# Kernel optimization log

Measured on AMD Instinct MI355X. Metric: run time of the kernel, lower is better.

Reference implementation:

```python
import jax, jax.numpy as jnp
import numpy as np
from jax import lax

NPOINT, RADIUS, NSAMPLE, K_KEY = 64, 1.0, 32, 64

def conv1d(x, W, b):
    # 1x1 Conv1d: x [B,Cin,N], W [Cout,Cin], b [Cout] -> [B,Cout,N]
    return jnp.einsum('bcn,dc->bdn', x, W) + b[None, :, None]

def farthest_point_sample(xyz, npoint):
    # xyz [B,N,3] -> idx [B,npoint]
    B, N, _ = xyz.shape
    dist0 = jnp.full((B, N), 1e10, dtype=xyz.dtype)
    far0 = jnp.zeros((B,), dtype=jnp.int32)
    def body(carry, _):
        dist, far = carry
        centroid = jnp.take_along_axis(xyz, far[:, None, None].astype(jnp.int32), axis=1)  # [B,1,3]
        d = jnp.sum((xyz - centroid) ** 2, -1)
        dist = jnp.minimum(dist, d)
        nxt = jnp.argmax(dist, -1).astype(jnp.int32)
        return (dist, nxt), far
    _, idxs = lax.scan(body, (dist0, far0), None, length=npoint)
    return idxs.T  # [B,npoint]

def ball_query(radius, nsample, xyz, new_xyz):
    # xyz [B,N,3], new_xyz [B,S,3] -> group_idx [B,S,nsample]
    N = xyz.shape[1]
    sqr = jnp.sum((new_xyz[:, :, None, :] - xyz[:, None, :, :]) ** 2, -1)  # [B,S,N]
    gidx = jnp.where(sqr > radius ** 2, N, jnp.arange(N, dtype=jnp.int32)[None, None, :])
    gidx = jnp.sort(gidx, axis=-1)[..., :nsample]
    first = gidx[..., :1]
    gidx = jnp.where(gidx == N, first, gidx)
    return gidx

def sample_and_group(npoint, radius, nsample, xyz, points):
    # xyz [B,N,3], points [B,N,D]
    B = xyz.shape[0]
    fps_idx = farthest_point_sample(xyz, npoint)                     # [B,S]
    bidx = jnp.arange(B)[:, None]
    new_xyz = xyz[bidx, fps_idx]                                     # [B,S,3]
    gidx = ball_query(radius, nsample, xyz, new_xyz)                 # [B,S,ns]
    bidx2 = jnp.arange(B)[:, None, None]
    grouped_xyz = xyz[bidx2, gidx]                                   # [B,S,ns,3]
    grouped_xyz_norm = grouped_xyz - new_xyz[:, :, None, :]
    grouped_points = points[bidx2, gidx]                             # [B,S,ns,D]
    new_points = jnp.concatenate([grouped_xyz_norm, grouped_points], axis=-1)
    return new_xyz, new_points

def setup_inputs() -> dict:
    key = jax.random.key(0)
    ks = jax.random.split(key, 12)
    B, C, N = 8, 6, 65536
    def w(k, co, ci):
        return jax.random.normal(k, (co, ci), jnp.float32) * (1.0 / np.sqrt(ci))
    return {
        'src_pts': jax.random.normal(ks[0], (B, C, N), jnp.float32),
        'tgt_pts': jax.random.normal(ks[1], (B, C, N), jnp.float32),
        'W1': w(ks[2], 32, 6),  'b1': jnp.zeros((32,), jnp.float32),
        'W2': w(ks[3], 64, 32), 'b2': jnp.zeros((64,), jnp.float32),
        'Wa': w(ks[4], 16, 64), 'ba': jnp.zeros((16,), jnp.float32),
        'Wb': w(ks[5], 8, 16),  'bb': jnp.zeros((8,), jnp.float32),
        'Wc': w(ks[6], 1, 8),   'bc': jnp.zeros((1,), jnp.float32),
    }

def reference(src_pts, tgt_pts, W1, b1, W2, b2, Wa, ba, Wb, bb, Wc, bc):
    # feat_extraction_layer: 1x1 conv stack over points -> deep per-point features
    h = jax.nn.relu(conv1d(src_pts, W1, b1))            # [B,32,N]
    deep_feat_pts = jax.nn.relu(conv1d(h, W2, b2))      # [B,64,N]
    # weighting_layer: per-point saliency weight + top-k keypoint indices (1-D, batch-0 idiom)
    w = jax.nn.relu(conv1d(deep_feat_pts, Wa, ba))
    w = jax.nn.relu(conv1d(w, Wb, bb))
    w = jax.nn.softplus(conv1d(w, Wc, bc))              # [B,1,N]
    _, keypts_idx = lax.top_k(w[0, 0], K_KEY)           # [K]
    # irregular keypoint gather (shared index across batch, as in src_pts[:, :, idx])
    src_keypts = src_pts[:, :, keypts_idx].transpose(0, 2, 1)   # [B,K,C]
    # ball-query sample_and_group on keypoints (computed then discarded, as in original)
    _gxyz, _gpts = sample_and_group(NPOINT, RADIUS, NSAMPLE, src_keypts[:, :, :3], src_keypts[:, :, 3:])
    return src_keypts
```

## Files before the change

kernel.cpp:

```cpp
#include <hip/hip_runtime.h>
#include <stdint.h>

#define N_PTS 65536
#define NB1 32768
#define NB2 4096
#define CAND_CAP 4096
#define FCAP 1024
typedef unsigned long long u64;


__global__ __launch_bounds__(256) void zero_kernel(uint4* __restrict__ z, int n4)
{
    const int i = blockIdx.x * 256 + threadIdx.x;
    const uint4 zz = {0u, 0u, 0u, 0u};
    if (i < n4) z[i] = zz;
}

__global__ __launch_bounds__(128, 1) void score_kernel(
    const float* __restrict__ src,
    const float* __restrict__ W1, const float* __restrict__ b1,
    const float* __restrict__ W2, const float* __restrict__ b2,
    const float* __restrict__ Wa, const float* __restrict__ ba,
    const float* __restrict__ Wb, const float* __restrict__ bb,
    const float* __restrict__ Wc, const float* __restrict__ bc,
    float* __restrict__ scores, unsigned* __restrict__ hist1)
{
    __shared__ unsigned histL[NB1];
    __shared__ __align__(16) float sW1[32 * 8];
    __shared__ __align__(16) float sW2[64 * 32];
    __shared__ __align__(16) float sWaT[64 * 16];
    __shared__ __align__(16) float sWb[8 * 16];
    __shared__ float sb2[64], sba[16], sbb[8], sWc[8], sbc1[1];
    const int t = threadIdx.x;

    {
        uint4* h4 = (uint4*)histL;
        const uint4 zz = {0u, 0u, 0u, 0u};
        #pragma unroll
        for (int i = 0; i < 64; i++) h4[t + 128 * i] = zz;
    }
    for (int i = t; i < 256; i += 128) {
        const int j = i >> 3, c = i & 7;
        sW1[i] = (c < 6) ? W1[j * 6 + c] : ((c == 6) ? b1[j] : 0.f);
    }
    for (int i = t; i < 2048; i += 128) sW2[i] = W2[i];
    for (int i = t; i < 1024; i += 128) {
        const int j = i >> 4, q = i & 15;
        sWaT[i] = Wa[q * 64 + j];
    }
    if (t < 128) sWb[t] = Wb[t];
    if (t < 64)  sb2[t] = b2[t];
    if (t < 16)  sba[t] = ba[t];
    if (t < 8)   { sbb[t] = bb[t]; sWc[t] = Wc[t]; }
    if (t == 0)  sbc1[0] = bc[0];
    __syncthreads();

    const int base = blockIdx.x * 512;
    int p[4];
    #pragma unroll
    for (int P = 0; P < 4; P++) p[P] = base + 128 * P + t;

    float x[4][6];
    #pragma unroll
    for (int c = 0; c < 6; c++) {
        #pragma unroll
        for (int P = 0; P < 4; P++) x[P][c] = src[c * N_PTS + p[P]];
    }

    float h1[4][32];
    #pragma unroll 8
    for (int j = 0; j < 32; j++) {
        const float4 wA = *(const float4*)&sW1[j * 8];
        const float4 wB = *(const float4*)&sW1[j * 8 + 4];
        #pragma unroll
        for (int P = 0; P < 4; P++) {
            float a = wB.z;
            a = fmaf(wA.x, x[P][0], a); a = fmaf(wA.y, x[P][1], a);
            a = fmaf(wA.z, x[P][2], a); a = fmaf(wA.w, x[P][3], a);
            a = fmaf(wB.x, x[P][4], a); a = fmaf(wB.y, x[P][5], a);
            h1[P][j] = fmaxf(a, 0.f);
        }
    }

    float h3[4][16];
    #pragma unroll
    for (int q = 0; q < 16; q++) {
        const float b = sba[q];
        h3[0][q] = b; h3[1][q] = b; h3[2][q] = b; h3[3][q] = b;
    }

    #pragma unroll 2
    for (int j = 0; j < 64; j++) {
        const float4* w2r = (const float4*)&sW2[j * 32];
        const float4* war = (const float4*)&sWaT[j * 16];
        float4 w[8], wq[4];
        #pragma unroll
        for (int i = 0; i < 8; i++) w[i] = w2r[i];
        #pragma unroll
        for (int i = 0; i < 4; i++) wq[i] = war[i];
        const float bj = sb2[j];

        float v[4];
        #pragma unroll
        for (int P = 0; P < 4; P++) {
            float a0 = 0.f, a1 = 0.f, a2 = 0.f, a3 = 0.f;
            #pragma unroll
            for (int i4 = 0; i4 < 8; i4++) {
                a0 = fmaf(w[i4].x, h1[P][4 * i4 + 0], a0);
                a1 = fmaf(w[i4].y, h1[P][4 * i4 + 1], a1);
                a2 = fmaf(w[i4].z, h1[P][4 * i4 + 2], a2);
                a3 = fmaf(w[i4].w, h1[P][4 * i4 + 3], a3);
            }
            v[P] = fmaxf((a0 + a1) + (a2 + a3) + bj, 0.f);
        }
        #pragma unroll
        for (int q4 = 0; q4 < 4; q4++) {
            const float4 ww = wq[q4];
            #pragma unroll
            for (int P = 0; P < 4; P++) {
                h3[P][4 * q4 + 0] = fmaf(ww.x, v[P], h3[P][4 * q4 + 0]);
                h3[P][4 * q4 + 1] = fmaf(ww.y, v[P], h3[P][4 * q4 + 1]);
                h3[P][4 * q4 + 2] = fmaf(ww.z, v[P], h3[P][4 * q4 + 2]);
                h3[P][4 * q4 + 3] = fmaf(ww.w, v[P], h3[P][4 * q4 + 3]);
            }
        }
    }
    #pragma unroll
    for (int q = 0; q < 16; q++) {
        #pragma unroll
        for (int P = 0; P < 4; P++) h3[P][q] = fmaxf(h3[P][q], 0.f);
    }

    float z[4] = { sbc1[0], sbc1[0], sbc1[0], sbc1[0] };
    #pragma unroll
    for (int j = 0; j < 8; j++) {
        const float4* wbr = (const float4*)&sWb[j * 16];
        const float4 w0 = wbr[0], w1 = wbr[1], w2 = wbr[2], w3 = wbr[3];
        const float bj = sbb[j], wc = sWc[j];
        #pragma unroll
        for (int P = 0; P < 4; P++) {
            float s0 = bj, s1 = 0.f, s2 = 0.f, s3 = 0.f;
            s0 = fmaf(w0.x, h3[P][0],  s0); s1 = fmaf(w0.y, h3[P][1],  s1);
            s2 = fmaf(w0.z, h3[P][2],  s2); s3 = fmaf(w0.w, h3[P][3],  s3);
            s0 = fmaf(w1.x, h3[P][4],  s0); s1 = fmaf(w1.y, h3[P][5],  s1);
            s2 = fmaf(w1.z, h3[P][6],  s2); s3 = fmaf(w1.w, h3[P][7],  s3);
            s0 = fmaf(w2.x, h3[P][8],  s0); s1 = fmaf(w2.y, h3[P][9],  s1);
            s2 = fmaf(w2.z, h3[P][10], s2); s3 = fmaf(w2.w, h3[P][11], s3);
            s0 = fmaf(w3.x, h3[P][12], s0); s1 = fmaf(w3.y, h3[P][13], s1);
            s2 = fmaf(w3.z, h3[P][14], s2); s3 = fmaf(w3.w, h3[P][15], s3);
            z[P] = fmaf(wc, fmaxf((s0 + s1) + (s2 + s3), 0.f), z[P]);
        }
    }

    #pragma unroll
    for (int P = 0; P < 4; P++) {
        const float sp = fmaxf(z[P], 0.f) + log1pf(expf(-fabsf(z[P])));
        scores[p[P]] = sp;
        atomicAdd(&histL[__float_as_uint(sp) >> 16], 1u);
    }
    __syncthreads();

    {
        const uint4* h4 = (const uint4*)histL;
        for (int i = t; i < NB1 / 4; i += 128) {
            const uint4 v = h4[i];
            if (v.x) atomicAdd(&hist1[4 * i + 0], v.x);
            if (v.y) atomicAdd(&hist1[4 * i + 1], v.y);
            if (v.z) atomicAdd(&hist1[4 * i + 2], v.z);
            if (v.w) atomicAdd(&hist1[4 * i + 3], v.w);
        }
    }
}

__global__ __launch_bounds__(256) void refine_kernel(
    const unsigned* __restrict__ hist1, const float* __restrict__ scores,
    unsigned* __restrict__ hist2, int* __restrict__ meta,
    u64* __restrict__ cand, const float* __restrict__ src,
    float* __restrict__ out)
{
    __shared__ unsigned csum[256];
    __shared__ unsigned bsum[128];
    __shared__ unsigned h2[NB2];
    __shared__ u64 keys[FCAP];
    __shared__ int idxs[64];
    __shared__ int sh_c, sh_B, sh_T2, sh_cnt;
    __shared__ unsigned sh_tail, sh_rank;
    const int t = threadIdx.x;

    {
        unsigned s = 0;
        const uint4* h4 = (const uint4*)(hist1 + t * 128);
        #pragma unroll
        for (int i = 0; i < 32; i++) {
            const uint4 v = h4[i];
            s += v.x + v.y + v.z + v.w;
        }
        csum[t] = s;
    }
    __syncthreads();
    for (int d = 1; d < 256; d <<= 1) {
        const unsigned v = (t + d < 256) ? csum[t + d] : 0u;
        __syncthreads();
        csum[t] += v;
        __syncthreads();
    }
    {
        const unsigned here = csum[t];
        const unsigned nxt = (t + 1 < 256) ? csum[t + 1] : 0u;
        if (here >= 64u && nxt < 64u) sh_c = t;
    }
    __syncthreads();
    const int cstar = sh_c;
    if (t < 128) bsum[t] = hist1[cstar * 128 + t];
    __syncthreads();
    {
        const unsigned ctail = (cstar + 1 < 256) ? csum[cstar + 1] : 0u;
        for (int d = 1; d < 128; d <<= 1) {
            unsigned v = 0u;
            if (t < 128 && t + d < 128) v = bsum[t + d];
            __syncthreads();
            if (t < 128) bsum[t] += v;
            __syncthreads();
        }
        if (t < 128) {
            const unsigned here = bsum[t] + ctail;
            const unsigned nxt = (t + 1 < 128) ? bsum[t + 1] + ctail : ctail;
            if (here >= 64u && nxt < 64u) { sh_B = cstar * 128 + t; sh_tail = nxt; }
        }
    }
    __syncthreads();
    const unsigned Bstar = (unsigned)sh_B;
    const unsigned tail1 = sh_tail;

    {
        const float4* s4 = (const float4*)scores;
        const int i = blockIdx.x * 256 + t;
        const float4 v = s4[i];
        const int n0 = 4 * i;
        #pragma unroll
        for (int k = 0; k < 4; k++) {
            const float sv = (k == 0) ? v.x : (k == 1) ? v.y : (k == 2) ? v.z : v.w;
            const unsigned b = __float_as_uint(sv);
            const unsigned hi = b >> 16;
            if (hi >= Bstar) {
                const int p = atomicAdd(&meta[2], 1);
                if (p < CAND_CAP) cand[p] = ((u64)b << 32) | (unsigned)~(n0 + k);
                if (hi == Bstar) atomicAdd(&hist2[(b & 0xFFFFu) >> 4], 1u);
            }
        }
    }

    __syncthreads();
    __threadfence();
    if (t == 0) sh_rank = atomicAdd((unsigned*)&meta[3], 1u);
    __syncthreads();
    if (sh_rank != 63u) return;
    __threadfence();

    {
        uint4* d = (uint4*)h2;
        const uint4* s = (const uint4*)hist2;
        #pragma unroll
        for (int i = 0; i < 4; i++) d[t + 256 * i] = s[t + 256 * i];
    }
    __syncthreads();

    {
        unsigned s = 0;
        #pragma unroll
        for (int i = 0; i < 16; i++) s += h2[t * 16 + i];
        csum[t] = s;
    }
    __syncthreads();
    for (int d = 1; d < 256; d <<= 1) {
        const unsigned v = (t + d < 256) ? csum[t + d] : 0u;
        __syncthreads();
        csum[t] += v;
        __syncthreads();
    }
    {
        const unsigned here = tail1 + csum[t];
        const unsigned nxt = tail1 + ((t + 1 < 256) ? csum[t + 1] : 0u);
        if (here >= 64u && nxt < 64u) sh_c = t;
    }
    __syncthreads();
    {
        const int c2 = sh_c;
        if (t == 0) {
            unsigned acc = tail1 + ((c2 + 1 < 256) ? csum[c2 + 1] : 0u);
            int T2 = c2 * 16;
            for (int b = c2 * 16 + 15; b >= c2 * 16; b--) {
                acc += h2[b];
                if (acc >= 64u) { T2 = b; break; }
            }
            sh_T2 = T2;
            sh_cnt = 0;
        }
    }
    __syncthreads();
    const unsigned T2 = (unsigned)sh_T2;

    int count = meta[2];
    if (count > CAND_CAP) count = CAND_CAP;
    for (int i = t; i < count; i += 256) {
        const u64 key = cand[i];
        const unsigned b = (unsigned)(key >> 32);
        const unsigned hi = b >> 16;
        if (hi > Bstar || ((b & 0xFFFFu) >> 4) >= T2) {
            const int p = atomicAdd(&sh_cnt, 1);
            if (p < FCAP) keys[p] = key;
        }
    }
    __syncthreads();

    int fcnt = sh_cnt;
    if (fcnt > FCAP) fcnt = FCAP;
    for (int i = t; i < fcnt; i += 256) {
        const u64 me = keys[i];
        int r = 0;
        for (int j = 0; j < fcnt; j++) r += (keys[j] > me);
        if (r < 64) idxs[r] = (int)~(unsigned)(me & 0xFFFFFFFFu);
    }
    __syncthreads();

    for (int e = t; e < 3072; e += 256) {
        const int b  = e / 384;
        const int rr = e % 384;
        const int kk = rr / 6;
        const int c  = rr % 6;
        out[e] = src[(b * 6 + c) * N_PTS + idxs[kk]];
    }
}

extern "C" void kernel_launch(void* const* d_in, const int* in_sizes, int n_in,
                              void* d_out, int out_size, void* d_ws, size_t ws_size,
                              hipStream_t stream)
{
    const float* src = (const float*)d_in[0];
    const float* W1 = (const float*)d_in[2];
    const float* b1 = (const float*)d_in[3];
    const float* W2 = (const float*)d_in[4];
    const float* b2 = (const float*)d_in[5];
    const float* Wa = (const float*)d_in[6];
    const float* ba = (const float*)d_in[7];
    const float* Wb = (const float*)d_in[8];
    const float* bb = (const float*)d_in[9];
    const float* Wc = (const float*)d_in[10];
    const float* bc = (const float*)d_in[11];

    char* ws = (char*)d_ws;
    float*    scores = (float*)ws;
    unsigned* hist1  = (unsigned*)(ws + 256 * 1024);
    unsigned* hist2  = (unsigned*)(ws + 384 * 1024);
    int*      meta   = (int*)(ws + 400 * 1024);
    u64*      cand   = (u64*)(ws + 408 * 1024);
    float*    out    = (float*)d_out;

    const int n4 = (NB1 + NB2 + 16) / 4;
    zero_kernel<<<(n4 + 255) / 256, 256, 0, stream>>>((uint4*)hist1, n4);
    score_kernel<<<128, 128, 0, stream>>>(src, W1, b1, W2, b2, Wa, ba,
                                          Wb, bb, Wc, bc, scores, hist1);
    refine_kernel<<<64, 256, 0, stream>>>(hist1, scores, hist2, meta, cand,
                                          src, out);
}
```

Baseline: 164.1 us.

## Split histogram and final selection into separate kernels, removing in-kernel last-block sync

Moves the 128KB shared histogram out of the score kernel into a dedicated hist_kernel, so the score kernel uses less LDS and no longer has to zero it or flush it with global atomics. The last-block-done pattern in refine_kernel (threadfence plus atomic counter) is replaced by a separate single-block final_kernel, with Bstar and tail passed through meta. This adds two kernel launches and an extra read of the scores array in exchange for a lighter score kernel and simpler synchronisation.

Measured after the change: 167.1 us. No clear change (+1.9%).

```diff
diff --git a/kernel.cpp b/kernel.cpp
--- a/kernel.cpp
+++ b/kernel.cpp
@@ -16,16 +16,17 @@
     if (i < n4) z[i] = zz;
 }
 
-__global__ __launch_bounds__(128, 1) void score_kernel(
+__global__ __launch_bounds__(128)
+__attribute__((amdgpu_waves_per_eu(1, 1)))
+void score_kernel(
     const float* __restrict__ src,
     const float* __restrict__ W1, const float* __restrict__ b1,
     const float* __restrict__ W2, const float* __restrict__ b2,
     const float* __restrict__ Wa, const float* __restrict__ ba,
     const float* __restrict__ Wb, const float* __restrict__ bb,
     const float* __restrict__ Wc, const float* __restrict__ bc,
-    float* __restrict__ scores, unsigned* __restrict__ hist1)
-{
-    __shared__ unsigned histL[NB1];
+    float* __restrict__ scores)
+{
     __shared__ __align__(16) float sW1[32 * 8];
     __shared__ __align__(16) float sW2[64 * 32];
     __shared__ __align__(16) float sWaT[64 * 16];
@@ -33,12 +34,6 @@
     __shared__ float sb2[64], sba[16], sbb[8], sWc[8], sbc1[1];
     const int t = threadIdx.x;
 
-    {
-        uint4* h4 = (uint4*)histL;
-        const uint4 zz = {0u, 0u, 0u, 0u};
-        #pragma unroll
-        for (int i = 0; i < 64; i++) h4[t + 128 * i] = zz;
-    }
     for (int i = t; i < 256; i += 128) {
         const int j = i >> 3, c = i & 7;
         sW1[i] = (c < 6) ? W1[j * 6 + c] : ((c == 6) ? b1[j] : 0.f);
@@ -156,35 +151,48 @@
     for (int P = 0; P < 4; P++) {
         const float sp = fmaxf(z[P], 0.f) + log1pf(expf(-fabsf(z[P])));
         scores[p[P]] = sp;
-        atomicAdd(&histL[__float_as_uint(sp) >> 16], 1u);
-    }
-    __syncthreads();
-
-    {
-        const uint4* h4 = (const uint4*)histL;
-        for (int i = t; i < NB1 / 4; i += 128) {
-            const uint4 v = h4[i];
-            if (v.x) atomicAdd(&hist1[4 * i + 0], v.x);
-            if (v.y) atomicAdd(&hist1[4 * i + 1], v.y);
-            if (v.z) atomicAdd(&hist1[4 * i + 2], v.z);
-            if (v.w) atomicAdd(&hist1[4 * i + 3], v.w);
-        }
+    }
+}
+
+__global__ __launch_bounds__(256) void hist_kernel(
+    const float* __restrict__ scores, unsigned* __restrict__ hist1)
+{
+    __shared__ unsigned histL[NB1];
+    const int t = threadIdx.x;
+    {
+        uint4* h4 = (uint4*)histL;
+        const uint4 zz = {0u, 0u, 0u, 0u};
+        #pragma unroll
+        for (int i = 0; i < 32; i++) h4[t + 256 * i] = zz;
+    }
+    __syncthreads();
+
+    const float4 v = ((const float4*)scores)[blockIdx.x * 256 + t];
+    atomicAdd(&histL[__float_as_uint(v.x) >> 16], 1u);
+    atomicAdd(&histL[__float_as_uint(v.y) >> 16], 1u);
+    atomicAdd(&histL[__float_as_uint(v.z) >> 16], 1u);
+    atomicAdd(&histL[__float_as_uint(v.w) >> 16], 1u);
+    __syncthreads();
+
+    const uint4* h4 = (const uint4*)histL;
+    for (int i = t; i < NB1 / 4; i += 256) {
+        const uint4 v2 = h4[i];
+        if (v2.x) atomicAdd(&hist1[4 * i + 0], v2.x);
+        if (v2.y) atomicAdd(&hist1[4 * i + 1], v2.y);
+        if (v2.z) atomicAdd(&hist1[4 * i + 2], v2.z);
+        if (v2.w) atomicAdd(&hist1[4 * i + 3], v2.w);
     }
 }
 
 __global__ __launch_bounds__(256) void refine_kernel(
     const unsigned* __restrict__ hist1, const float* __restrict__ scores,
     unsigned* __restrict__ hist2, int* __restrict__ meta,
-    u64* __restrict__ cand, const float* __restrict__ src,
-    float* __restrict__ out)
+    u64* __restrict__ cand)
 {
     __shared__ unsigned csum[256];
     __shared__ unsigned bsum[128];
-    __shared__ unsigned h2[NB2];
-    __shared__ u64 keys[FCAP];
-    __shared__ int idxs[64];
-    __shared__ int sh_c, sh_B, sh_T2, sh_cnt;
-    __shared__ unsigned sh_tail, sh_rank;
+    __shared__ int sh_c, sh_B;
+    __shared__ unsigned sh_tail;
     const int t = threadIdx.x;
 
     {
@@ -230,32 +238,38 @@
     }
     __syncthreads();
     const unsigned Bstar = (unsigned)sh_B;
-    const unsigned tail1 = sh_tail;
-
-    {
-        const float4* s4 = (const float4*)scores;
-        const int i = blockIdx.x * 256 + t;
-        const float4 v = s4[i];
-        const int n0 = 4 * i;
-        #pragma unroll
-        for (int k = 0; k < 4; k++) {
-            const float sv = (k == 0) ? v.x : (k == 1) ? v.y : (k == 2) ? v.z : v.w;
-            const unsigned b = __float_as_uint(sv);
-            const unsigned hi = b >> 16;
-            if (hi >= Bstar) {
-                const int p = atomicAdd(&meta[2], 1);
-                if (p < CAND_CAP) cand[p] = ((u64)b << 32) | (unsigned)~(n0 + k);
-                if (hi == Bstar) atomicAdd(&hist2[(b & 0xFFFFu) >> 4], 1u);
-            }
-        }
-    }
-
-    __syncthreads();
-    __threadfence();
-    if (t == 0) sh_rank = atomicAdd((unsigned*)&meta[3], 1u);
-    __syncthreads();
-    if (sh_rank != 63u) return;
-    __threadfence();
+    if (blockIdx.x == 0 && t == 0) { meta[0] = sh_B; meta[1] = (int)sh_tail; }
+
+    const float4* s4 = (const float4*)scores;
+    const int i = blockIdx.x * 256 + t;
+    const float4 v = s4[i];
+    const int n0 = 4 * i;
+    #pragma unroll
+    for (int k = 0; k < 4; k++) {
+        const float sv = (k == 0) ? v.x : (k == 1) ? v.y : (k == 2) ? v.z : v.w;
+        const unsigned b = __float_as_uint(sv);
+        const unsigned hi = b >> 16;
+        if (hi >= Bstar) {
+            const int p = atomicAdd(&meta[2], 1);
+            if (p < CAND_CAP) cand[p] = ((u64)b << 32) | (unsigned)~(n0 + k);
+            if (hi == Bstar) atomicAdd(&hist2[(b & 0xFFFFu) >> 4], 1u);
+        }
+    }
+}
+
+__global__ __launch_bounds__(256) void final_kernel(
+    const unsigned* __restrict__ hist2, const int* __restrict__ meta,
+    const u64* __restrict__ cand, const float* __restrict__ src,
+    float* __restrict__ out)
+{
+    __shared__ unsigned h2[NB2];
+    __shared__ unsigned csum[256];
+    __shared__ u64 keys[FCAP];
+    __shared__ int idxs[64];
+    __shared__ int sh_c, sh_T2, sh_cnt;
+    const int t = threadIdx.x;
+    const unsigned Bstar = (unsigned)meta[0];
+    const unsigned tail1 = (unsigned)meta[1];
 
     {
         uint4* d = (uint4*)h2;
@@ -359,7 +373,8 @@
     const int n4 = (NB1 + NB2 + 16) / 4;
     zero_kernel<<<(n4 + 255) / 256, 256, 0, stream>>>((uint4*)hist1, n4);
     score_kernel<<<128, 128, 0, stream>>>(src, W1, b1, W2, b2, Wa, ba,
-                                          Wb, bb, Wc, bc, scores, hist1);
-    refine_kernel<<<64, 256, 0, stream>>>(hist1, scores, hist2, meta, cand,
-                                          src, out);
-}
+                                          Wb, bb, Wc, bc, scores);
+    hist_kernel<<<64, 256, 0, stream>>>(scores, hist1);
+    refine_kernel<<<64, 256, 0, stream>>>(hist1, scores, hist2, meta, cand);
+    final_kernel<<<1, 256, 0, stream>>>(hist2, meta, cand, src, out);
+}
```
